# Optimization experiments

Hardware: AMD Instinct MI355X
Metric: run time of the kernel (lower is better)

The kernel has to match this reference:

```python
import jax, jax.numpy as jnp
import numpy as np

N_NODES = 50000
N_EDGES = 800000
IN_DIM, HID, N_CLS = 128, 128, 64


def setup_inputs() -> dict:
    key = jax.random.key(0)
    ks = jax.random.split(key, 10)
    x = jax.random.normal(ks[0], (N_NODES, IN_DIM), dtype=jnp.float32)
    src = jax.random.randint(ks[1], (N_EDGES,), 0, N_NODES, dtype=jnp.int32)
    dst = jax.random.randint(ks[2], (N_EDGES,), 0, N_NODES, dtype=jnp.int32)
    def lin(k, fi, fo):
        s = 1.0 / np.sqrt(fi)
        return jax.random.uniform(k, (fi, fo), jnp.float32, -s, s)
    # layer dims: 128->128, 128->128, 128->64 (num_layers=2 -> 3 SAGEConv layers)
    params = {
        'W_self0': lin(ks[3], IN_DIM, HID), 'W_neigh0': lin(ks[4], IN_DIM, HID),
        'b0': jnp.zeros((HID,), jnp.float32),
        'W_self1': lin(ks[5], HID, HID), 'W_neigh1': lin(ks[6], HID, HID),
        'b1': jnp.zeros((HID,), jnp.float32),
        'W_self2': lin(ks[7], HID, N_CLS), 'W_neigh2': lin(ks[8], HID, N_CLS),
        'b2': jnp.zeros((N_CLS,), jnp.float32),
    }
    return {'x': x, 'src': src, 'dst': dst, **params}


def _sage_layer(h, src, dst, W_self, W_neigh, b):
    # mean aggregator: gather source features, segment-sum into dst, divide by in-degree
    msg = h[src]                                                   # [E, d]
    agg = jax.ops.segment_sum(msg, dst, num_segments=N_NODES)      # [N, d]
    deg = jax.ops.segment_sum(jnp.ones((src.shape[0],), h.dtype), dst,
                              num_segments=N_NODES)
    h_neigh = agg / jnp.maximum(deg, 1.0)[:, None]
    return h @ W_self + h_neigh @ W_neigh + b


def reference(x, src, dst, W_self0, W_neigh0, b0, W_self1, W_neigh1, b1,
              W_self2, W_neigh2, b2):
    h = _sage_layer(x, src, dst, W_self0, W_neigh0, b0)
    h = jax.nn.relu(h)
    h = _sage_layer(h, src, dst, W_self1, W_neigh1, b1)
    h = jax.nn.relu(h)
    h = _sage_layer(h, src, dst, W_self2, W_neigh2, b2)
    return h
```

## Files before the change

kernel.cpp:

```cpp
#include <hip/hip_runtime.h>
#include <hip/hip_bf16.h>


#define NFEAT 128
#define SLOTS 64

typedef __attribute__((ext_vector_type(8))) short short8;
typedef __attribute__((ext_vector_type(4))) float floatx4;

__device__ __forceinline__ float bf_lo(unsigned u) { return __uint_as_float(u << 16); }
__device__ __forceinline__ float bf_hi(unsigned u) { return __uint_as_float(u & 0xffff0000u); }
__device__ __forceinline__ ushort f2bf(float f) {
    __hip_bfloat16 h = __float2bfloat16(f);
    return *(ushort*)&h;
}
__device__ __forceinline__ unsigned pack2(float a, float b) {
    return (unsigned)f2bf(a) | ((unsigned)f2bf(b) << 16);
}


__global__ __launch_bounds__(256) void k_prep(
    const int* __restrict__ dst, int* __restrict__ deg, int* __restrict__ slotpos,
    int E, int NN,
    const float* __restrict__ X, ushort* __restrict__ X16, int n2,
    const float* __restrict__ Ws0, const float* __restrict__ Wn0,
    const float* __restrict__ Ws1, const float* __restrict__ Wn1,
    const float* __restrict__ Ws2, const float* __restrict__ Wn2,
    ushort* __restrict__ Wt0, ushort* __restrict__ Wt1, ushort* __restrict__ Wt2,
    int e8b, int cvtb) {
    int b = blockIdx.x, t = threadIdx.x;
    if (b < e8b) {
        int base = (b * 256 + t) * 8;
        if (base + 8 <= E) {
            int4 da = *(const int4*)(dst + base);
            int4 db = *(const int4*)(dst + base + 4);
            int4 pa, pb;
            pa.x = (da.x << 6) | atomicAdd(&deg[da.x], 1);
            pa.y = (da.y << 6) | atomicAdd(&deg[da.y], 1);
            pa.z = (da.z << 6) | atomicAdd(&deg[da.z], 1);
            pa.w = (da.w << 6) | atomicAdd(&deg[da.w], 1);
            pb.x = (db.x << 6) | atomicAdd(&deg[db.x], 1);
            pb.y = (db.y << 6) | atomicAdd(&deg[db.y], 1);
            pb.z = (db.z << 6) | atomicAdd(&deg[db.z], 1);
            pb.w = (db.w << 6) | atomicAdd(&deg[db.w], 1);
            *(int4*)(slotpos + base) = pa;
            *(int4*)(slotpos + base + 4) = pb;
        } else {
            for (int e = base; e < E; ++e) {
                int d = dst[e];
                slotpos[e] = (d << 6) | atomicAdd(&deg[d], 1);
            }
        }
    } else if (b < e8b + cvtb) {
        int i = (b - e8b) * 256 + t;
        if (i < n2) {
            float2 v = ((const float2*)X)[i];
            ((unsigned*)X16)[i] = pack2(v.x, v.y);
        }
    } else {
        int idx = (b - e8b - cvtb) * 256 + t;
        if (idx < 32768) {
            int n = idx >> 8, k = idx & 255;
            Wt0[idx] = f2bf(k < 128 ? Ws0[k * 128 + n] : Wn0[(k - 128) * 128 + n]);
        } else if (idx < 65536) {
            int l = idx - 32768, n = l >> 8, k = l & 255;
            Wt1[l] = f2bf(k < 128 ? Ws1[k * 128 + n] : Wn1[(k - 128) * 128 + n]);
        } else if (idx < 81920) {
            int l = idx - 65536, n = l >> 8, k = l & 255;
            Wt2[l] = f2bf(k < 128 ? Ws2[k * 64 + n] : Wn2[(k - 128) * 64 + n]);
        }
    }
}


__global__ __launch_bounds__(256) void k_scatter(const int* __restrict__ src,
                                                 const int* __restrict__ slotpos,
                                                 int* __restrict__ csr, int E) {
    int base = (blockIdx.x * 256 + threadIdx.x) * 8;
    if (base + 8 <= E) {
        int4 pa = *(const int4*)(slotpos + base);
        int4 pb = *(const int4*)(slotpos + base + 4);
        int4 sa = *(const int4*)(src + base);
        int4 sb = *(const int4*)(src + base + 4);
        csr[pa.x] = sa.x; csr[pa.y] = sa.y; csr[pa.z] = sa.z; csr[pa.w] = sa.w;
        csr[pb.x] = sb.x; csr[pb.y] = sb.y; csr[pb.z] = sb.z; csr[pb.w] = sb.w;
    } else {
        for (int e = base; e < E; ++e) csr[slotpos[e]] = src[e];
    }
}


template <int FEAT, bool OUT_BF16>
__global__ __launch_bounds__(256) void k_agg_p(const ushort* __restrict__ H,
                                               const int* __restrict__ deg,
                                               const int* __restrict__ csr,
                                               void* __restrict__ outp, int NN) {
    constexpr int LPR = FEAT / 8;
    constexpr int EPG = 64 / LPR;
    constexpr int NS = 8;
    int lane = threadIdx.x & 63, wid = threadIdx.x >> 6;
    int sub = lane / LPR, fl = lane % LPR;
    int wstr = gridDim.x * 4;
    int node = blockIdx.x * 4 + wid;

    int d_cur = 0;
    int s_cur[NS];
    if (node < NN) {
        d_cur = deg[node];
        const int* slot = csr + (node << 6);
#pragma unroll
        for (int k = 0; k < NS; ++k) s_cur[k] = slot[k * EPG + sub];
    }

    while (node < NN) {
        int nnode = node + wstr;
        int d_nxt = 0;
        int s_nxt[NS];
        if (nnode < NN) {
            d_nxt = deg[nnode];
            const int* slot2 = csr + (nnode << 6);
#pragma unroll
            for (int k = 0; k < NS; ++k) s_nxt[k] = slot2[k * EPG + sub];
        }

        int dd = d_cur;
        int d = (dd < SLOTS) ? dd : SLOTS;
        float acc[8] = {};
        uint4 v[NS];
#pragma unroll
        for (int k = 0; k < NS; ++k) {
            int e = k * EPG + sub;
            v[k] = make_uint4(0, 0, 0, 0);
            if (e < d) v[k] = *(const uint4*)(H + (size_t)s_cur[k] * FEAT + fl * 8);
        }
#pragma unroll
        for (int k = 0; k < NS; ++k) {
            acc[0] += bf_lo(v[k].x); acc[1] += bf_hi(v[k].x);
            acc[2] += bf_lo(v[k].y); acc[3] += bf_hi(v[k].y);
            acc[4] += bf_lo(v[k].z); acc[5] += bf_hi(v[k].z);
            acc[6] += bf_lo(v[k].w); acc[7] += bf_hi(v[k].w);
        }
        if constexpr (NS * EPG < SLOTS) {
            if (d > NS * EPG) {
                const int* slot = csr + (node << 6);
                for (int e = NS * EPG + sub; e < d; e += EPG) {
                    int r = slot[e];
                    uint4 vv = *(const uint4*)(H + (size_t)r * FEAT + fl * 8);
                    acc[0] += bf_lo(vv.x); acc[1] += bf_hi(vv.x);
                    acc[2] += bf_lo(vv.y); acc[3] += bf_hi(vv.y);
                    acc[4] += bf_lo(vv.z); acc[5] += bf_hi(vv.z);
                    acc[6] += bf_lo(vv.w); acc[7] += bf_hi(vv.w);
                }
            }
        }
#pragma unroll
        for (int off = LPR; off < 64; off <<= 1)
#pragma unroll
            for (int i = 0; i < 8; ++i) acc[i] += __shfl_xor(acc[i], off, 64);
        if (sub == 0) {
            float inv = (dd > 0) ? 1.0f / (float)dd : 0.0f;
            if constexpr (OUT_BF16) {
                unsigned u[4];
#pragma unroll
                for (int i = 0; i < 4; ++i)
                    u[i] = pack2(acc[2 * i] * inv, acc[2 * i + 1] * inv);
                *(uint4*)((ushort*)outp + (size_t)node * FEAT + fl * 8) =
                    make_uint4(u[0], u[1], u[2], u[3]);
            } else {
                float* O = (float*)outp;
                size_t b = (size_t)node * FEAT + fl * 8;
#pragma unroll
                for (int i = 0; i < 8; ++i) O[b + i] = acc[i] * inv;
            }
        }
        node = nnode;
        d_cur = d_nxt;
#pragma unroll
        for (int k = 0; k < NS; ++k) s_cur[k] = s_nxt[k];
    }
}


template <int BM, int BN, int NKB, bool SPLIT, bool OUT_BF16>
__global__ __launch_bounds__(2 * (BN / 64) * 64) void gemm_mfma(
    const ushort* __restrict__ Hs, const ushort* __restrict__ Ag,
    const ushort* __restrict__ Wt, int ldw, const float* __restrict__ bias,
    const float* __restrict__ addin, void* __restrict__ Cout, int M, int relu) {
    constexpr int NW = BN / 64;
    constexpr int NTHR = 2 * NW * 64;
    constexpr int MT = BM / 32;
    constexpr int LDA = 40;
    __shared__ ushort Asl[BM * LDA];
    __shared__ ushort Bsl[BN * LDA];

    int t = threadIdx.x;
    int lane = t & 63;
    int wid = t >> 6;
    int wm = wid & 1, wn = wid >> 1;
    int l15 = lane & 15, quad = lane >> 4;
    int m0 = blockIdx.x * BM;

    floatx4 acc[MT][4] = {};

    for (int kb = 0; kb < NKB; ++kb) {
        const ushort* Asrc;
        int kOff;
        if constexpr (SPLIT) {
            Asrc = (kb < NKB / 2) ? Hs : Ag;
            kOff = (kb & (NKB / 2 - 1)) * 32;
        } else {
            Asrc = Hs;
            kOff = kb * 32;
        }
        __syncthreads();
#pragma unroll
        for (int id = t; id < BM * 4; id += NTHR) {
            int r = id >> 2, p = id & 3;
            uint4 v = make_uint4(0, 0, 0, 0);
            if (m0 + r < M) v = *(const uint4*)(Asrc + (size_t)(m0 + r) * NFEAT + kOff + p * 8);
            *(uint4*)(&Asl[r * LDA + p * 8]) = v;
        }
#pragma unroll
        for (int id = t; id < BN * 4; id += NTHR) {
            int r = id >> 2, p = id & 3;
            uint4 v = *(const uint4*)(Wt + (size_t)r * ldw + kb * 32 + p * 8);
            *(uint4*)(&Bsl[r * LDA + p * 8]) = v;
        }
        __syncthreads();

        short8 a[MT], b[4];
#pragma unroll
        for (int mt = 0; mt < MT; ++mt)
            a[mt] = *(const short8*)(&Asl[(wm * (MT * 16) + mt * 16 + l15) * LDA + quad * 8]);
#pragma unroll
        for (int nt = 0; nt < 4; ++nt)
            b[nt] = *(const short8*)(&Bsl[(wn * 64 + nt * 16 + l15) * LDA + quad * 8]);
#pragma unroll
        for (int mt = 0; mt < MT; ++mt)
#pragma unroll
            for (int nt = 0; nt < 4; ++nt)
                acc[mt][nt] = __builtin_amdgcn_mfma_f32_16x16x32_bf16(a[mt], b[nt], acc[mt][nt], 0, 0, 0);
    }

#pragma unroll
    for (int mt = 0; mt < MT; ++mt) {
        int mbase = m0 + wm * (MT * 16) + mt * 16 + quad * 4;
#pragma unroll
        for (int nt = 0; nt < 4; ++nt) {
            int col = wn * 64 + nt * 16 + l15;
            float bv = bias ? bias[col] : 0.0f;
#pragma unroll
            for (int r = 0; r < 4; ++r) {
                int m = mbase + r;
                if (m < M) {
                    float v = acc[mt][nt][r] + bv;
                    if (addin) v += addin[(size_t)m * BN + col];
                    if (relu) v = fmaxf(v, 0.f);
                    if constexpr (OUT_BF16) {
                        ((unsigned short*)Cout)[(size_t)m * BN + col] = f2bf(v);
                    } else {
                        ((float*)Cout)[(size_t)m * BN + col] = v;
                    }
                }
            }
        }
    }
}


static inline size_t align_up(size_t x) { return (x + 255) & ~(size_t)255; }

extern "C" void kernel_launch(void* const* d_in, const int* in_sizes, int n_in,
                              void* d_out, int out_size, void* d_ws, size_t ws_size,
                              hipStream_t stream) {
    const float* x   = (const float*)d_in[0];
    const int*   src = (const int*)d_in[1];
    const int*   dst = (const int*)d_in[2];
    const float* Ws0 = (const float*)d_in[3];
    const float* Wn0 = (const float*)d_in[4];
    const float* b0  = (const float*)d_in[5];
    const float* Ws1 = (const float*)d_in[6];
    const float* Wn1 = (const float*)d_in[7];
    const float* b1  = (const float*)d_in[8];
    const float* Ws2 = (const float*)d_in[9];
    const float* Wn2 = (const float*)d_in[10];
    const float* b2  = (const float*)d_in[11];
    float* out = (float*)d_out;

    const int NN = in_sizes[0] / NFEAT;
    const int E  = in_sizes[1];

    char* w = (char*)d_ws;
    ushort* X16  = (ushort*)w; w += align_up((size_t)NN * NFEAT * 2);
    ushort* Ha   = (ushort*)w; w += align_up((size_t)NN * NFEAT * 2);
    ushort* Hb   = (ushort*)w; w += align_up((size_t)NN * NFEAT * 2);
    ushort* AGG  = (ushort*)w; w += align_up((size_t)NN * NFEAT * 2);
    ushort* Wt0  = (ushort*)w; w += align_up((size_t)128 * 256 * 2);
    ushort* Wt1  = (ushort*)w; w += align_up((size_t)128 * 256 * 2);
    ushort* Wt2  = (ushort*)w; w += align_up((size_t)64 * 256 * 2);
    int* deg     = (int*)w;    w += align_up((size_t)NN * 4);
    int* csr     = (int*)w;    w += align_up((size_t)NN * SLOTS * 4);

    int*    slotpos = (int*)Ha;
    ushort* G2  = X16;
    float*  A2  = (float*)AGG;

    hipMemsetAsync(deg, 0, (size_t)NN * 4, stream);

    const int e8b  = (E / 8 + 255) / 256;
    const int n2   = NN * NFEAT / 2;
    const int cvtb = (n2 + 255) / 256;
    const int wb   = (81920 + 255) / 256;

    k_prep<<<e8b + cvtb + wb, 256, 0, stream>>>(
        dst, deg, slotpos, E, NN, x, X16, n2,
        Ws0, Wn0, Ws1, Wn1, Ws2, Wn2, Wt0, Wt1, Wt2, e8b, cvtb);
    k_scatter<<<e8b, 256, 0, stream>>>(src, slotpos, csr, E);

    const int agb  = 2048;
    const int gm64 = (NN + 63) / 64;

    k_agg_p<128, true><<<agb, 256, 0, stream>>>(X16, deg, csr, AGG, NN);
    gemm_mfma<64, 128, 8, true, true><<<gm64, 256, 0, stream>>>(X16, AGG, Wt0, 256, b0, nullptr, Ha, NN, 1);

    k_agg_p<128, true><<<agb, 256, 0, stream>>>(Ha, deg, csr, AGG, NN);
    gemm_mfma<64, 128, 8, true, true><<<gm64, 256, 0, stream>>>(Ha, AGG, Wt1, 256, b1, nullptr, Hb, NN, 1);

    gemm_mfma<64, 64, 4, false, true><<<gm64, 128, 0, stream>>>(Hb, nullptr, Wt2 + 128, 256, nullptr, nullptr, G2, NN, 0);
    k_agg_p<64, false><<<agb, 256, 0, stream>>>(G2, deg, csr, A2, NN);
    gemm_mfma<64, 64, 4, false, false><<<gm64, 128, 0, stream>>>(Hb, nullptr, Wt2, 256, b2, A2, out, NN, 0);
}
```

Baseline: 283.9 us.

## Split self/neighbor GEMMs and co-schedule independent stages in fused launches

Each layer's GEMM is split into a self-projection, written as an fp32 partial, and a neighbor-projection that adds that partial. The independent self GEMM is then merged into the same launch as the CSR scatter (layer 0) or the aggregation (layer 1), so the blocks can overlap. The last layer's two GEMMs share one launch, and the final aggregation accumulates straight into the output instead of going through a separate add GEMM. The aim is fewer dependent launches and better overlap of memory-bound gathers with compute, at the cost of an extra fp32 partial buffer round-trip to memory.

```diff
diff --git a/kernel.cpp b/kernel.cpp
--- a/kernel.cpp
+++ b/kernel.cpp
@@ -73,10 +73,10 @@
 }
 
 
-__global__ __launch_bounds__(256) void k_scatter(const int* __restrict__ src,
-                                                 const int* __restrict__ slotpos,
-                                                 int* __restrict__ csr, int E) {
-    int base = (blockIdx.x * 256 + threadIdx.x) * 8;
+__device__ __forceinline__ void scatter_body(int bid, int t, const int* __restrict__ src,
+                                             const int* __restrict__ slotpos,
+                                             int* __restrict__ csr, int E) {
+    int base = (bid * 256 + t) * 8;
     if (base + 8 <= E) {
         int4 pa = *(const int4*)(slotpos + base);
         int4 pb = *(const int4*)(slotpos + base + 4);
@@ -89,103 +89,11 @@
     }
 }
 
-
-template <int FEAT, bool OUT_BF16>
-__global__ __launch_bounds__(256) void k_agg_p(const ushort* __restrict__ H,
-                                               const int* __restrict__ deg,
-                                               const int* __restrict__ csr,
-                                               void* __restrict__ outp, int NN) {
-    constexpr int LPR = FEAT / 8;
-    constexpr int EPG = 64 / LPR;
-    constexpr int NS = 8;
-    int lane = threadIdx.x & 63, wid = threadIdx.x >> 6;
-    int sub = lane / LPR, fl = lane % LPR;
-    int wstr = gridDim.x * 4;
-    int node = blockIdx.x * 4 + wid;
-
-    int d_cur = 0;
-    int s_cur[NS];
-    if (node < NN) {
-        d_cur = deg[node];
-        const int* slot = csr + (node << 6);
-#pragma unroll
-        for (int k = 0; k < NS; ++k) s_cur[k] = slot[k * EPG + sub];
-    }
-
-    while (node < NN) {
-        int nnode = node + wstr;
-        int d_nxt = 0;
-        int s_nxt[NS];
-        if (nnode < NN) {
-            d_nxt = deg[nnode];
-            const int* slot2 = csr + (nnode << 6);
-#pragma unroll
-            for (int k = 0; k < NS; ++k) s_nxt[k] = slot2[k * EPG + sub];
-        }
-
-        int dd = d_cur;
-        int d = (dd < SLOTS) ? dd : SLOTS;
-        float acc[8] = {};
-        uint4 v[NS];
-#pragma unroll
-        for (int k = 0; k < NS; ++k) {
-            int e = k * EPG + sub;
-            v[k] = make_uint4(0, 0, 0, 0);
-            if (e < d) v[k] = *(const uint4*)(H + (size_t)s_cur[k] * FEAT + fl * 8);
-        }
-#pragma unroll
-        for (int k = 0; k < NS; ++k) {
-            acc[0] += bf_lo(v[k].x); acc[1] += bf_hi(v[k].x);
-            acc[2] += bf_lo(v[k].y); acc[3] += bf_hi(v[k].y);
-            acc[4] += bf_lo(v[k].z); acc[5] += bf_hi(v[k].z);
-            acc[6] += bf_lo(v[k].w); acc[7] += bf_hi(v[k].w);
-        }
-        if constexpr (NS * EPG < SLOTS) {
-            if (d > NS * EPG) {
-                const int* slot = csr + (node << 6);
-                for (int e = NS * EPG + sub; e < d; e += EPG) {
-                    int r = slot[e];
-                    uint4 vv = *(const uint4*)(H + (size_t)r * FEAT + fl * 8);
-                    acc[0] += bf_lo(vv.x); acc[1] += bf_hi(vv.x);
-                    acc[2] += bf_lo(vv.y); acc[3] += bf_hi(vv.y);
-                    acc[4] += bf_lo(vv.z); acc[5] += bf_hi(vv.z);
-                    acc[6] += bf_lo(vv.w); acc[7] += bf_hi(vv.w);
-                }
-            }
-        }
-#pragma unroll
-        for (int off = LPR; off < 64; off <<= 1)
-#pragma unroll
-            for (int i = 0; i < 8; ++i) acc[i] += __shfl_xor(acc[i], off, 64);
-        if (sub == 0) {
-            float inv = (dd > 0) ? 1.0f / (float)dd : 0.0f;
-            if constexpr (OUT_BF16) {
-                unsigned u[4];
-#pragma unroll
-                for (int i = 0; i < 4; ++i)
-                    u[i] = pack2(acc[2 * i] * inv, acc[2 * i + 1] * inv);
-                *(uint4*)((ushort*)outp + (size_t)node * FEAT + fl * 8) =
-                    make_uint4(u[0], u[1], u[2], u[3]);
-            } else {
-                float* O = (float*)outp;
-                size_t b = (size_t)node * FEAT + fl * 8;
-#pragma unroll
-                for (int i = 0; i < 8; ++i) O[b + i] = acc[i] * inv;
-            }
-        }
-        node = nnode;
-        d_cur = d_nxt;
-#pragma unroll
-        for (int k = 0; k < NS; ++k) s_cur[k] = s_nxt[k];
-    }
-}
-
-
-template <int BM, int BN, int NKB, bool SPLIT, bool OUT_BF16>
-__global__ __launch_bounds__(2 * (BN / 64) * 64) void gemm_mfma(
-    const ushort* __restrict__ Hs, const ushort* __restrict__ Ag,
-    const ushort* __restrict__ Wt, int ldw, const float* __restrict__ bias,
-    const float* __restrict__ addin, void* __restrict__ Cout, int M, int relu) {
+template <int BM, int BN, int NKB, bool OUT_BF16>
+__device__ __forceinline__ void gemm_body(int bid, int t,
+    const ushort* __restrict__ Hs, const ushort* __restrict__ Wt, int ldw,
+    const float* __restrict__ bias, const float* __restrict__ addin,
+    void* __restrict__ Cout, int M, int relu) {
     constexpr int NW = BN / 64;
     constexpr int NTHR = 2 * NW * 64;
     constexpr int MT = BM / 32;
@@ -193,31 +101,21 @@
     __shared__ ushort Asl[BM * LDA];
     __shared__ ushort Bsl[BN * LDA];
 
-    int t = threadIdx.x;
     int lane = t & 63;
     int wid = t >> 6;
     int wm = wid & 1, wn = wid >> 1;
     int l15 = lane & 15, quad = lane >> 4;
-    int m0 = blockIdx.x * BM;
+    int m0 = bid * BM;
 
     floatx4 acc[MT][4] = {};
 
     for (int kb = 0; kb < NKB; ++kb) {
-        const ushort* Asrc;
-        int kOff;
-        if constexpr (SPLIT) {
-            Asrc = (kb < NKB / 2) ? Hs : Ag;
-            kOff = (kb & (NKB / 2 - 1)) * 32;
-        } else {
-            Asrc = Hs;
-            kOff = kb * 32;
-        }
         __syncthreads();
 #pragma unroll
         for (int id = t; id < BM * 4; id += NTHR) {
             int r = id >> 2, p = id & 3;
             uint4 v = make_uint4(0, 0, 0, 0);
-            if (m0 + r < M) v = *(const uint4*)(Asrc + (size_t)(m0 + r) * NFEAT + kOff + p * 8);
+            if (m0 + r < M) v = *(const uint4*)(Hs + (size_t)(m0 + r) * NFEAT + kb * 32 + p * 8);
             *(uint4*)(&Asl[r * LDA + p * 8]) = v;
         }
 #pragma unroll
@@ -265,6 +163,151 @@
             }
         }
     }
+}
+
+template <int FEAT, int MODE>
+__device__ __forceinline__ void agg_body(int vbid, int nb, int t,
+    const ushort* __restrict__ H, const int* __restrict__ deg,
+    const int* __restrict__ csr, void* __restrict__ outp, int NN) {
+    constexpr int LPR = FEAT / 8;
+    constexpr int EPG = 64 / LPR;
+    constexpr int NS = 8;
+    int lane = t & 63, wid = t >> 6;
+    int sub = lane / LPR, fl = lane % LPR;
+    int wstr = nb * 4;
+    int node = vbid * 4 + wid;
+
+    int d_cur = 0;
+    int s_cur[NS];
+    if (node < NN) {
+        d_cur = deg[node];
+        const int* slot = csr + (node << 6);
+#pragma unroll
+        for (int k = 0; k < NS; ++k) s_cur[k] = slot[k * EPG + sub];
+    }
+
+    while (node < NN) {
+        int nnode = node + wstr;
+        int d_nxt = 0;
+        int s_nxt[NS];
+        if (nnode < NN) {
+            d_nxt = deg[nnode];
+            const int* slot2 = csr + (nnode << 6);
+#pragma unroll
+            for (int k = 0; k < NS; ++k) s_nxt[k] = slot2[k * EPG + sub];
+        }
+
+        int dd = d_cur;
+        int d = (dd < SLOTS) ? dd : SLOTS;
+        float acc[8] = {};
+        uint4 v[NS];
+#pragma unroll
+        for (int k = 0; k < NS; ++k) {
+            int e = k * EPG + sub;
+            v[k] = make_uint4(0, 0, 0, 0);
+            if (e < d) v[k] = *(const uint4*)(H + (size_t)s_cur[k] * FEAT + fl * 8);
+        }
+#pragma unroll
+        for (int k = 0; k < NS; ++k) {
+            acc[0] += bf_lo(v[k].x); acc[1] += bf_hi(v[k].x);
+            acc[2] += bf_lo(v[k].y); acc[3] += bf_hi(v[k].y);
+            acc[4] += bf_lo(v[k].z); acc[5] += bf_hi(v[k].z);
+            acc[6] += bf_lo(v[k].w); acc[7] += bf_hi(v[k].w);
+        }
+        if constexpr (NS * EPG < SLOTS) {
+            if (d > NS * EPG) {
+                const int* slot = csr + (node << 6);
+                for (int e = NS * EPG + sub; e < d; e += EPG) {
+                    int r = slot[e];
+                    uint4 vv = *(const uint4*)(H + (size_t)r * FEAT + fl * 8);
+                    acc[0] += bf_lo(vv.x); acc[1] += bf_hi(vv.x);
+                    acc[2] += bf_lo(vv.y); acc[3] += bf_hi(vv.y);
+                    acc[4] += bf_lo(vv.z); acc[5] += bf_hi(vv.z);
+                    acc[6] += bf_lo(vv.w); acc[7] += bf_hi(vv.w);
+                }
+            }
+        }
+#pragma unroll
+        for (int off = LPR; off < 64; off <<= 1)
+#pragma unroll
+            for (int i = 0; i < 8; ++i) acc[i] += __shfl_xor(acc[i], off, 64);
+        if (sub == 0) {
+            float inv = (dd > 0) ? 1.0f / (float)dd : 0.0f;
+            if constexpr (MODE == 0) {
+                unsigned u[4];
+#pragma unroll
+                for (int i = 0; i < 4; ++i)
+                    u[i] = pack2(acc[2 * i] * inv, acc[2 * i + 1] * inv);
+                *(uint4*)((ushort*)outp + (size_t)node * FEAT + fl * 8) =
+                    make_uint4(u[0], u[1], u[2], u[3]);
+            } else {
+                float* O = (float*)outp;
+                size_t b = (size_t)node * FEAT + fl * 8;
+#pragma unroll
+                for (int i = 0; i < 8; ++i) O[b + i] += acc[i] * inv;
+            }
+        }
+        node = nnode;
+        d_cur = d_nxt;
+#pragma unroll
+        for (int k = 0; k < NS; ++k) s_cur[k] = s_nxt[k];
+    }
+}
+
+
+__global__ __launch_bounds__(256) void k_d2(
+    const int* __restrict__ src, const int* __restrict__ slotpos,
+    int* __restrict__ csr, int E, int sb,
+    const ushort* __restrict__ X16, const ushort* __restrict__ Wt0,
+    const float* __restrict__ b0, float* __restrict__ CP, int M) {
+    if ((int)blockIdx.x < sb)
+        scatter_body(blockIdx.x, threadIdx.x, src, slotpos, csr, E);
+    else
+        gemm_body<64, 128, 4, false>(blockIdx.x - sb, threadIdx.x,
+                                     X16, Wt0, 256, b0, nullptr, CP, M, 0);
+}
+
+__global__ __launch_bounds__(256) void k_agg128(
+    const ushort* __restrict__ H, const int* __restrict__ deg,
+    const int* __restrict__ csr, void* __restrict__ outp, int NN) {
+    agg_body<128, 0>(blockIdx.x, gridDim.x, threadIdx.x, H, deg, csr, outp, NN);
+}
+
+__global__ __launch_bounds__(256) void k_ngemm(
+    const ushort* __restrict__ AGG, const ushort* __restrict__ Wtn,
+    const float* __restrict__ CP, ushort* __restrict__ Hout, int M) {
+    gemm_body<64, 128, 4, true>(blockIdx.x, threadIdx.x,
+                                AGG, Wtn, 256, nullptr, CP, Hout, M, 1);
+}
+
+__global__ __launch_bounds__(256) void k_d5(
+    const ushort* __restrict__ Ha, const int* __restrict__ deg,
+    const int* __restrict__ csr, void* __restrict__ AGG, int NN, int agb,
+    const ushort* __restrict__ Wt1, const float* __restrict__ b1,
+    float* __restrict__ CP, int M) {
+    if ((int)blockIdx.x < agb)
+        agg_body<128, 0>(blockIdx.x, agb, threadIdx.x, Ha, deg, csr, AGG, NN);
+    else
+        gemm_body<64, 128, 4, false>(blockIdx.x - agb, threadIdx.x,
+                                     Ha, Wt1, 256, b1, nullptr, CP, M, 0);
+}
+
+__global__ __launch_bounds__(128) void k_d7(
+    const ushort* __restrict__ Hb, const ushort* __restrict__ Wt2,
+    const float* __restrict__ b2, ushort* __restrict__ G2,
+    float* __restrict__ out, int M, int pb) {
+    if ((int)blockIdx.x < pb)
+        gemm_body<64, 64, 4, true>(blockIdx.x, threadIdx.x,
+                                   Hb, Wt2 + 128, 256, nullptr, nullptr, G2, M, 0);
+    else
+        gemm_body<64, 64, 4, false>(blockIdx.x - pb, threadIdx.x,
+                                    Hb, Wt2, 256, b2, nullptr, out, M, 0);
+}
+
+__global__ __launch_bounds__(256) void k_aggacc(
+    const ushort* __restrict__ G2, const int* __restrict__ deg,
+    const int* __restrict__ csr, float* __restrict__ out, int NN) {
+    agg_body<64, 2>(blockIdx.x, gridDim.x, threadIdx.x, G2, deg, csr, out, NN);
 }
 
 
@@ -295,6 +338,7 @@
     ushort* Ha   = (ushort*)w; w += align_up((size_t)NN * NFEAT * 2);
     ushort* Hb   = (ushort*)w; w += align_up((size_t)NN * NFEAT * 2);
     ushort* AGG  = (ushort*)w; w += align_up((size_t)NN * NFEAT * 2);
+    float*  CP   = (float*)w;  w += align_up((size_t)NN * NFEAT * 4);
     ushort* Wt0  = (ushort*)w; w += align_up((size_t)128 * 256 * 2);
     ushort* Wt1  = (ushort*)w; w += align_up((size_t)128 * 256 * 2);
     ushort* Wt2  = (ushort*)w; w += align_up((size_t)64 * 256 * 2);
@@ -303,7 +347,6 @@
 
     int*    slotpos = (int*)Ha;
     ushort* G2  = X16;
-    float*  A2  = (float*)AGG;
 
     hipMemsetAsync(deg, 0, (size_t)NN * 4, stream);
 
@@ -311,22 +354,22 @@
     const int n2   = NN * NFEAT / 2;
     const int cvtb = (n2 + 255) / 256;
     const int wb   = (81920 + 255) / 256;
+    const int gm   = (NN + 63) / 64;
+    const int agb  = 2048;
+    const int agbm = 1536;
 
     k_prep<<<e8b + cvtb + wb, 256, 0, stream>>>(
         dst, deg, slotpos, E, NN, x, X16, n2,
         Ws0, Wn0, Ws1, Wn1, Ws2, Wn2, Wt0, Wt1, Wt2, e8b, cvtb);
-    k_scatter<<<e8b, 256, 0, stream>>>(src, slotpos, csr, E);
-
-    const int agb  = 2048;
-    const int gm64 = (NN + 63) / 64;
-
-    k_agg_p<128, true><<<agb, 256, 0, stream>>>(X16, deg, csr, AGG, NN);
-    gemm_mfma<64, 128, 8, true, true><<<gm64, 256, 0, stream>>>(X16, AGG, Wt0, 256, b0, nullptr, Ha, NN, 1);
-
-    k_agg_p<128, true><<<agb, 256, 0, stream>>>(Ha, deg, csr, AGG, NN);
-    gemm_mfma<64, 128, 8, true, true><<<gm64, 256, 0, stream>>>(Ha, AGG, Wt1, 256, b1, nullptr, Hb, NN, 1);
-
-    gemm_mfma<64, 64, 4, false, true><<<gm64, 128, 0, stream>>>(Hb, nullptr, Wt2 + 128, 256, nullptr, nullptr, G2, NN, 0);
-    k_agg_p<64, false><<<agb, 256, 0, stream>>>(G2, deg, csr, A2, NN);
-    gemm_mfma<64, 64, 4, false, false><<<gm64, 128, 0, stream>>>(Hb, nullptr, Wt2, 256, b2, A2, out, NN, 0);
-}
+
+    k_d2<<<e8b + gm, 256, 0, stream>>>(src, slotpos, csr, E, e8b, X16, Wt0, b0, CP, NN);
+
+    k_agg128<<<agb, 256, 0, stream>>>(X16, deg, csr, AGG, NN);
+    k_ngemm<<<gm, 256, 0, stream>>>(AGG, Wt0 + 128, CP, Ha, NN);
+
+    k_d5<<<agbm + gm, 256, 0, stream>>>(Ha, deg, csr, AGG, NN, agbm, Wt1, b1, CP, NN);
+    k_ngemm<<<gm, 256, 0, stream>>>(AGG, Wt1 + 128, CP, Hb, NN);
+
+    k_d7<<<gm * 2, 128, 0, stream>>>(Hb, Wt2, b2, G2, out, NN, gm);
+    k_aggacc<<<agb, 256, 0, stream>>>(G2, deg, csr, out, NN);
+}
```

New measurement: 294.2 us. 3.6% more time.
